# Optimization experiments

Measured on AMD Instinct MI355X. Metric: run time of the kernel, lower is better.

Reference implementation:

```python
import jax, jax.numpy as jnp
import numpy as np


def setup_inputs() -> dict:
    key = jax.random.key(0)
    k1, k2 = jax.random.split(key)
    B, D, NUM_CLASSES = 8192, 128, 100
    features = jax.random.normal(k1, (B, D), dtype=jnp.float32)
    labels = jax.random.randint(k2, (B,), 0, NUM_CLASSES, dtype=jnp.int64)
    return {"features": features, "labels": labels}


def reference(features, labels):
    # temperature=0.07, clamp(min=0.01) -> 0.07
    TEMP = 0.07
    B = features.shape[0]
    dt = features.dtype

    # positive mask from labels: [B, B]
    mask = (labels[:, None] == labels[None, :]).astype(dt)

    # L2 normalize rows (F.normalize: x / max(||x||, eps))
    norm = jnp.sqrt(jnp.sum(features * features, axis=1, keepdims=True))
    f = features / jnp.maximum(norm, 1e-8)

    # similarity matrix, scaled and clamped to [-10, 10]
    sim = jnp.clip(jnp.matmul(f, f.T) / TEMP, -10.0, 10.0)

    eye = jnp.eye(B, dtype=dt)
    exp_sim = jnp.exp(sim)

    pos_sum = jnp.maximum(jnp.sum(exp_sim * (mask - eye), axis=1), 1e-8)
    neg_sum = jnp.maximum(jnp.sum(exp_sim * (1.0 - eye), axis=1), 1e-8)

    loss = -jnp.log(pos_sum / neg_sum)
    # NaN guard as in the original (returns 0 if any NaN)
    return jnp.where(jnp.any(jnp.isnan(loss)), jnp.zeros((), dt), jnp.mean(loss))
```

## Files before the change

### kernel.cpp

```cpp
#include <hip/hip_runtime.h>
#include <hip/hip_bf16.h>


using floatx4 = __attribute__((ext_vector_type(4))) float;
using intx4   = __attribute__((ext_vector_type(4))) int;
using intx8   = __attribute__((ext_vector_type(8))) int;
using llong2  = __attribute__((ext_vector_type(2))) long long;

constexpr int   Bn = 8192;
constexpr int   Dk = 128;
constexpr int   NSLICE = 32;
constexpr int   NBLK   = 32 * 32;
constexpr float PRESCALE = 4.5398160f;
constexpr float LN2      = 0.69314718056f;
constexpr int   SCALE1   = 0x7F7F7F7F;

__global__ __launch_bounds__(256) void normalize_k(
    const float* __restrict__ feat, unsigned char* __restrict__ fb,
    float* __restrict__ rowpos, float* __restrict__ rowneg,
    unsigned int* __restrict__ done) {
  if (blockIdx.x < 32) {
    rowpos[blockIdx.x * 256 + threadIdx.x] = 0.f;
    rowneg[blockIdx.x * 256 + threadIdx.x] = 0.f;
  }
  if (blockIdx.x == 32 && threadIdx.x == 0) *done = 0u;
  const int row  = blockIdx.x * 4 + (threadIdx.x >> 6);
  const int lane = threadIdx.x & 63;
  const float2 v = ((const float2*)(feat + (size_t)row * Dk))[lane];
  float s = v.x * v.x + v.y * v.y;
#pragma unroll
  for (int m = 1; m < 64; m <<= 1) s += __shfl_xor(s, m);
  const float inv = PRESCALE / fmaxf(sqrtf(s), 1e-8f);
  const int packed = __builtin_amdgcn_cvt_pk_fp8_f32(v.x * inv, v.y * inv, 0, false);
  const int k0 = 2 * lane;
  const int p  = ((k0 & 31) >> 3) * 32 + (k0 >> 5) * 8 + (k0 & 7);
  *(unsigned short*)(fb + (size_t)row * Dk + p) = (unsigned short)(packed & 0xffff);
}

__global__ __launch_bounds__(256, 2) void simloss_k(
    const unsigned char* __restrict__ fb, const int* __restrict__ labels,
    float* __restrict__ rowpos, float* __restrict__ rowneg,
    unsigned int* __restrict__ done, float* __restrict__ out) {
  __shared__ __align__(16) unsigned char Bsh[256 * Dk];

  const int t     = threadIdx.x;
  const int lane  = t & 63;
  const int wave  = t >> 6;
  const int quad  = lane >> 4;
  const int lr    = lane & 15;
  const int jbase = blockIdx.x * 256;

  {
    const int chunk = t & 7;
    const int r0    = t >> 3;
#pragma unroll
    for (int it = 0; it < 8; ++it) {
      const int row = r0 + it * 32;
      const llong2 v = *(const llong2*)(fb + (size_t)(jbase + row) * Dk + chunk * 16);
      *(llong2*)(Bsh + row * Dk + ((chunk ^ (row & 7)) * 16)) = v;
    }
  }

  int labj16[8];
#pragma unroll
  for (int j = 0; j < 8; ++j) {
    const int l0 = labels[jbase + (2 * j) * 16 + lr];
    const int l1 = labels[jbase + (2 * j + 1) * 16 + lr];
    labj16[j] = l0 | (l1 << 16);
  }

  bool dl[4];
#pragma unroll
  for (int r = 0; r < 4; ++r) dl[r] = (quad * 4 + r) == lr;

  const int sw  = lr & 7;
  const int ch0 = ((quad * 2)     ^ sw) * 16;
  const int ch1 = ((quad * 2 + 1) ^ sw) * 16;

  __syncthreads();

#pragma unroll 1
  for (int p = 0; p < 2; ++p) {
    const int ibase = blockIdx.y * 256 + wave * 64 + p * 32;

    intx8 A0, A1;
    {
      const unsigned char* ap0 = fb + (size_t)(ibase + lr) * Dk + quad * 32;
      A0 = *(const intx8*)(ap0);
      A1 = *(const intx8*)(ap0 + 16 * Dk);
    }

    int li[2][4];
#pragma unroll
    for (int tt = 0; tt < 2; ++tt)
#pragma unroll
      for (int r = 0; r < 4; ++r)
        li[tt][r] = labels[ibase + tt * 16 + quad * 4 + r];

    float pos[2][4] = {};
    float neg[2][4] = {};

#pragma unroll
    for (int jt = 0; jt < 16; ++jt) {
      const unsigned char* bp = Bsh + (jt * 16 + lr) * Dk;
      const intx4 Blo = *(const intx4*)(bp + ch0);
      const intx4 Bhi = *(const intx4*)(bp + ch1);
      intx8 Bv;
      Bv[0] = Blo[0]; Bv[1] = Blo[1]; Bv[2] = Blo[2]; Bv[3] = Blo[3];
      Bv[4] = Bhi[0]; Bv[5] = Bhi[1]; Bv[6] = Bhi[2]; Bv[7] = Bhi[3];

      floatx4 acc0 = {0.f, 0.f, 0.f, 0.f};
      floatx4 acc1 = {0.f, 0.f, 0.f, 0.f};
      acc0 = __builtin_amdgcn_mfma_scale_f32_16x16x128_f8f6f4(
          A0, Bv, acc0, 0, 0, 0, SCALE1, 0, SCALE1);
      acc1 = __builtin_amdgcn_mfma_scale_f32_16x16x128_f8f6f4(
          A1, Bv, acc1, 0, 0, 0, SCALE1, 0, SCALE1);

      const int j0 = jbase + jt * 16;
      const int lj = (jt & 1) ? (labj16[jt >> 1] >> 16) : (labj16[jt >> 1] & 0xffff);
      float e0, e1, e2, e3;
      e0 = __builtin_amdgcn_exp2f(acc0[0]);
      e1 = __builtin_amdgcn_exp2f(acc0[1]);
      e2 = __builtin_amdgcn_exp2f(acc0[2]);
      e3 = __builtin_amdgcn_exp2f(acc0[3]);
      if (j0 == ibase) {
        if (dl[0]) e0 = 0.f;
        if (dl[1]) e1 = 0.f;
        if (dl[2]) e2 = 0.f;
        if (dl[3]) e3 = 0.f;
      }
      neg[0][0] += e0; neg[0][1] += e1; neg[0][2] += e2; neg[0][3] += e3;
      pos[0][0] += (li[0][0] == lj) ? e0 : 0.f;
      pos[0][1] += (li[0][1] == lj) ? e1 : 0.f;
      pos[0][2] += (li[0][2] == lj) ? e2 : 0.f;
      pos[0][3] += (li[0][3] == lj) ? e3 : 0.f;
      e0 = __builtin_amdgcn_exp2f(acc1[0]);
      e1 = __builtin_amdgcn_exp2f(acc1[1]);
      e2 = __builtin_amdgcn_exp2f(acc1[2]);
      e3 = __builtin_amdgcn_exp2f(acc1[3]);
      if (j0 == ibase + 16) {
        if (dl[0]) e0 = 0.f;
        if (dl[1]) e1 = 0.f;
        if (dl[2]) e2 = 0.f;
        if (dl[3]) e3 = 0.f;
      }
      neg[1][0] += e0; neg[1][1] += e1; neg[1][2] += e2; neg[1][3] += e3;
      pos[1][0] += (li[1][0] == lj) ? e0 : 0.f;
      pos[1][1] += (li[1][1] == lj) ? e1 : 0.f;
      pos[1][2] += (li[1][2] == lj) ? e2 : 0.f;
      pos[1][3] += (li[1][3] == lj) ? e3 : 0.f;
    }

#pragma unroll
    for (int tt = 0; tt < 2; ++tt)
#pragma unroll
      for (int r = 0; r < 4; ++r) {
        float p2 = pos[tt][r], n2 = neg[tt][r];
#pragma unroll
        for (int m = 1; m < 16; m <<= 1) {
          p2 += __shfl_xor(p2, m);
          n2 += __shfl_xor(n2, m);
        }
        if (lr == 0) {
          const int row = ibase + tt * 16 + quad * 4 + r;
          atomicAdd(&rowpos[row], p2);
          atomicAdd(&rowneg[row], n2);
        }
      }

    __builtin_amdgcn_sched_barrier(0);
  }

  __syncthreads();
  int* flag = (int*)Bsh;
  if (t == 0) {
    __threadfence();
    const unsigned int old = atomicAdd(done, 1u);
    *flag = (old == (unsigned)(NBLK - 1)) ? 1 : 0;
  }
  __syncthreads();
  if (*flag) {
    __threadfence();
    const float4* rp4 = (const float4*)rowpos;
    const float4* rn4 = (const float4*)rowneg;
    float4 p4[8], n4[8];
#pragma unroll
    for (int z = 0; z < 8; ++z) p4[z] = rp4[t * 8 + z];
#pragma unroll
    for (int z = 0; z < 8; ++z) n4[z] = rn4[t * 8 + z];
    float acc = 0.f;
#pragma unroll
    for (int z = 0; z < 8; ++z) {
      acc += __builtin_amdgcn_logf(fmaxf(n4[z].x, 1e-8f)) - __builtin_amdgcn_logf(fmaxf(p4[z].x, 1e-8f));
      acc += __builtin_amdgcn_logf(fmaxf(n4[z].y, 1e-8f)) - __builtin_amdgcn_logf(fmaxf(p4[z].y, 1e-8f));
      acc += __builtin_amdgcn_logf(fmaxf(n4[z].z, 1e-8f)) - __builtin_amdgcn_logf(fmaxf(p4[z].z, 1e-8f));
      acc += __builtin_amdgcn_logf(fmaxf(n4[z].w, 1e-8f)) - __builtin_amdgcn_logf(fmaxf(p4[z].w, 1e-8f));
    }
#pragma unroll
    for (int m = 1; m < 64; m <<= 1) acc += __shfl_xor(acc, m);
    float* red = (float*)Bsh + 16;
    if (lane == 0) red[wave] = acc;
    __syncthreads();
    if (t == 0)
      *out = (red[0] + red[1] + red[2] + red[3]) * (LN2 / (float)Bn);
  }
}

extern "C" void kernel_launch(void* const* d_in, const int* in_sizes, int n_in,
                              void* d_out, int out_size, void* d_ws, size_t ws_size,
                              hipStream_t stream) {
  const float* feat   = (const float*)d_in[0];
  const int*   labels = (const int*)d_in[1];
  float* out = (float*)d_out;

  unsigned char* fb = (unsigned char*)d_ws;
  float* rowpos = (float*)((char*)d_ws + (size_t)Bn * Dk);
  float* rowneg = rowpos + Bn;
  unsigned int* done = (unsigned int*)(rowneg + Bn);

  normalize_k<<<Bn / 4, 256, 0, stream>>>(feat, fb, rowpos, rowneg, done);
  dim3 grid(NSLICE, 32);
  simloss_k<<<grid, 256, 0, stream>>>(fb, labels, rowpos, rowneg, done, out);
}
```

Measured before the change: 96.21 us.

## Software-pipeline MFMA with exp epilogue, specialize diagonal blocks, raise occupancy

Restructures the inner tile loop so the next MFMA pair is issued before the previous tile's exp/accumulate epilogue runs, overlapping matrix-core latency with the VALU work. The diagonal-masking logic is moved into a template and compiled only for blocks on the diagonal, so off-diagonal blocks skip the compares. Launch bounds are raised from 2 to 4 blocks per CU for more latency hiding. Keeping both accumulator pairs live costs extra registers, and the higher occupancy target may force spills.

```diff
diff --git a/kernel.cpp b/kernel.cpp
--- a/kernel.cpp
+++ b/kernel.cpp
@@ -37,7 +37,127 @@
   *(unsigned short*)(fb + (size_t)row * Dk + p) = (unsigned short)(packed & 0xffff);
 }
 
-__global__ __launch_bounds__(256, 2) void simloss_k(
+struct Lab16 { int w[8]; };
+
+template <bool DIAG>
+__device__ __forceinline__ void sim_pass(
+    const int ibase, const unsigned char* __restrict__ fb,
+    const int* __restrict__ labels, const unsigned char* __restrict__ Bsh,
+    float* __restrict__ rowpos, float* __restrict__ rowneg,
+    const int jbase, const int quad, const int lr,
+    const int ch0, const int ch1, const Lab16 LJ) {
+
+  intx8 A0, A1;
+  {
+    const unsigned char* ap0 = fb + (size_t)(ibase + lr) * Dk + quad * 32;
+    A0 = *(const intx8*)(ap0);
+    A1 = *(const intx8*)(ap0 + 16 * Dk);
+  }
+
+  int li[2][4];
+#pragma unroll
+  for (int tt = 0; tt < 2; ++tt)
+#pragma unroll
+    for (int r = 0; r < 4; ++r)
+      li[tt][r] = labels[ibase + tt * 16 + quad * 4 + r];
+
+  bool dl[4] = {false, false, false, false};
+  if (DIAG) {
+#pragma unroll
+    for (int r = 0; r < 4; ++r) dl[r] = (quad * 4 + r) == lr;
+  }
+
+  float pos[2][4] = {};
+  float neg[2][4] = {};
+
+  auto loadB = [&](int jt) -> intx8 {
+    const unsigned char* bp = Bsh + (jt * 16 + lr) * Dk;
+    const intx4 Blo = *(const intx4*)(bp + ch0);
+    const intx4 Bhi = *(const intx4*)(bp + ch1);
+    intx8 Bv;
+    Bv[0] = Blo[0]; Bv[1] = Blo[1]; Bv[2] = Blo[2]; Bv[3] = Blo[3];
+    Bv[4] = Bhi[0]; Bv[5] = Bhi[1]; Bv[6] = Bhi[2]; Bv[7] = Bhi[3];
+    return Bv;
+  };
+
+  auto consume = [&](const floatx4 c0, const floatx4 c1, int jt) {
+    const int j0 = jbase + jt * 16;
+    const int lj = (jt & 1) ? (LJ.w[jt >> 1] >> 16) : (LJ.w[jt >> 1] & 0xffff);
+    float e0, e1, e2, e3;
+    e0 = __builtin_amdgcn_exp2f(c0[0]);
+    e1 = __builtin_amdgcn_exp2f(c0[1]);
+    e2 = __builtin_amdgcn_exp2f(c0[2]);
+    e3 = __builtin_amdgcn_exp2f(c0[3]);
+    if (DIAG) {
+      if (j0 == ibase) {
+        if (dl[0]) e0 = 0.f;
+        if (dl[1]) e1 = 0.f;
+        if (dl[2]) e2 = 0.f;
+        if (dl[3]) e3 = 0.f;
+      }
+    }
+    neg[0][0] += e0; neg[0][1] += e1; neg[0][2] += e2; neg[0][3] += e3;
+    pos[0][0] += (li[0][0] == lj) ? e0 : 0.f;
+    pos[0][1] += (li[0][1] == lj) ? e1 : 0.f;
+    pos[0][2] += (li[0][2] == lj) ? e2 : 0.f;
+    pos[0][3] += (li[0][3] == lj) ? e3 : 0.f;
+    e0 = __builtin_amdgcn_exp2f(c1[0]);
+    e1 = __builtin_amdgcn_exp2f(c1[1]);
+    e2 = __builtin_amdgcn_exp2f(c1[2]);
+    e3 = __builtin_amdgcn_exp2f(c1[3]);
+    if (DIAG) {
+      if (j0 == ibase + 16) {
+        if (dl[0]) e0 = 0.f;
+        if (dl[1]) e1 = 0.f;
+        if (dl[2]) e2 = 0.f;
+        if (dl[3]) e3 = 0.f;
+      }
+    }
+    neg[1][0] += e0; neg[1][1] += e1; neg[1][2] += e2; neg[1][3] += e3;
+    pos[1][0] += (li[1][0] == lj) ? e0 : 0.f;
+    pos[1][1] += (li[1][1] == lj) ? e1 : 0.f;
+    pos[1][2] += (li[1][2] == lj) ? e2 : 0.f;
+    pos[1][3] += (li[1][3] == lj) ? e3 : 0.f;
+  };
+
+  const floatx4 z = {0.f, 0.f, 0.f, 0.f};
+
+  intx8 B0 = loadB(0);
+  floatx4 ac0 = __builtin_amdgcn_mfma_scale_f32_16x16x128_f8f6f4(
+      A0, B0, z, 0, 0, 0, SCALE1, 0, SCALE1);
+  floatx4 ac1 = __builtin_amdgcn_mfma_scale_f32_16x16x128_f8f6f4(
+      A1, B0, z, 0, 0, 0, SCALE1, 0, SCALE1);
+#pragma unroll
+  for (int jt = 0; jt < 15; ++jt) {
+    const intx8 Bv = loadB(jt + 1);
+    const floatx4 an0 = __builtin_amdgcn_mfma_scale_f32_16x16x128_f8f6f4(
+        A0, Bv, z, 0, 0, 0, SCALE1, 0, SCALE1);
+    const floatx4 an1 = __builtin_amdgcn_mfma_scale_f32_16x16x128_f8f6f4(
+        A1, Bv, z, 0, 0, 0, SCALE1, 0, SCALE1);
+    consume(ac0, ac1, jt);
+    ac0 = an0; ac1 = an1;
+  }
+  consume(ac0, ac1, 15);
+
+#pragma unroll
+  for (int tt = 0; tt < 2; ++tt)
+#pragma unroll
+    for (int r = 0; r < 4; ++r) {
+      float p2 = pos[tt][r], n2 = neg[tt][r];
+#pragma unroll
+      for (int m = 1; m < 16; m <<= 1) {
+        p2 += __shfl_xor(p2, m);
+        n2 += __shfl_xor(n2, m);
+      }
+      if (lr == 0) {
+        const int row = ibase + tt * 16 + quad * 4 + r;
+        atomicAdd(&rowpos[row], p2);
+        atomicAdd(&rowneg[row], n2);
+      }
+    }
+}
+
+__global__ __launch_bounds__(256, 4) void simloss_k(
     const unsigned char* __restrict__ fb, const int* __restrict__ labels,
     float* __restrict__ rowpos, float* __restrict__ rowneg,
     unsigned int* __restrict__ done, float* __restrict__ out) {
@@ -61,17 +181,13 @@
     }
   }
 
-  int labj16[8];
+  Lab16 LJ;
 #pragma unroll
   for (int j = 0; j < 8; ++j) {
     const int l0 = labels[jbase + (2 * j) * 16 + lr];
     const int l1 = labels[jbase + (2 * j + 1) * 16 + lr];
-    labj16[j] = l0 | (l1 << 16);
-  }
-
-  bool dl[4];
-#pragma unroll
-  for (int r = 0; r < 4; ++r) dl[r] = (quad * 4 + r) == lr;
+    LJ.w[j] = l0 | (l1 << 16);
+  }
 
   const int sw  = lr & 7;
   const int ch0 = ((quad * 2)     ^ sw) * 16;
@@ -79,96 +195,22 @@
 
   __syncthreads();
 
+  const int ib0 = blockIdx.y * 256 + wave * 64;
+
+  if (blockIdx.x == blockIdx.y) {
 #pragma unroll 1
-  for (int p = 0; p < 2; ++p) {
-    const int ibase = blockIdx.y * 256 + wave * 64 + p * 32;
-
-    intx8 A0, A1;
-    {
-      const unsigned char* ap0 = fb + (size_t)(ibase + lr) * Dk + quad * 32;
-      A0 = *(const intx8*)(ap0);
-      A1 = *(const intx8*)(ap0 + 16 * Dk);
-    }
-
-    int li[2][4];
-#pragma unroll
-    for (int tt = 0; tt < 2; ++tt)
-#pragma unroll
-      for (int r = 0; r < 4; ++r)
-        li[tt][r] = labels[ibase + tt * 16 + quad * 4 + r];
-
-    float pos[2][4] = {};
-    float neg[2][4] = {};
-
-#pragma unroll
-    for (int jt = 0; jt < 16; ++jt) {
-      const unsigned char* bp = Bsh + (jt * 16 + lr) * Dk;
-      const intx4 Blo = *(const intx4*)(bp + ch0);
-      const intx4 Bhi = *(const intx4*)(bp + ch1);
-      intx8 Bv;
-      Bv[0] = Blo[0]; Bv[1] = Blo[1]; Bv[2] = Blo[2]; Bv[3] = Blo[3];
-      Bv[4] = Bhi[0]; Bv[5] = Bhi[1]; Bv[6] = Bhi[2]; Bv[7] = Bhi[3];
-
-      floatx4 acc0 = {0.f, 0.f, 0.f, 0.f};
-      floatx4 acc1 = {0.f, 0.f, 0.f, 0.f};
-      acc0 = __builtin_amdgcn_mfma_scale_f32_16x16x128_f8f6f4(
-          A0, Bv, acc0, 0, 0, 0, SCALE1, 0, SCALE1);
-      acc1 = __builtin_amdgcn_mfma_scale_f32_16x16x128_f8f6f4(
-          A1, Bv, acc1, 0, 0, 0, SCALE1, 0, SCALE1);
-
-      const int j0 = jbase + jt * 16;
-      const int lj = (jt & 1) ? (labj16[jt >> 1] >> 16) : (labj16[jt >> 1] & 0xffff);
-      float e0, e1, e2, e3;
-      e0 = __builtin_amdgcn_exp2f(acc0[0]);
-      e1 = __builtin_amdgcn_exp2f(acc0[1]);
-      e2 = __builtin_amdgcn_exp2f(acc0[2]);
-      e3 = __builtin_amdgcn_exp2f(acc0[3]);
-      if (j0 == ibase) {
-        if (dl[0]) e0 = 0.f;
-        if (dl[1]) e1 = 0.f;
-        if (dl[2]) e2 = 0.f;
-        if (dl[3]) e3 = 0.f;
-      }
-      neg[0][0] += e0; neg[0][1] += e1; neg[0][2] += e2; neg[0][3] += e3;
-      pos[0][0] += (li[0][0] == lj) ? e0 : 0.f;
-      pos[0][1] += (li[0][1] == lj) ? e1 : 0.f;
-      pos[0][2] += (li[0][2] == lj) ? e2 : 0.f;
-      pos[0][3] += (li[0][3] == lj) ? e3 : 0.f;
-      e0 = __builtin_amdgcn_exp2f(acc1[0]);
-      e1 = __builtin_amdgcn_exp2f(acc1[1]);
-      e2 = __builtin_amdgcn_exp2f(acc1[2]);
-      e3 = __builtin_amdgcn_exp2f(acc1[3]);
-      if (j0 == ibase + 16) {
-        if (dl[0]) e0 = 0.f;
-        if (dl[1]) e1 = 0.f;
-        if (dl[2]) e2 = 0.f;
-        if (dl[3]) e3 = 0.f;
-      }
-      neg[1][0] += e0; neg[1][1] += e1; neg[1][2] += e2; neg[1][3] += e3;
-      pos[1][0] += (li[1][0] == lj) ? e0 : 0.f;
-      pos[1][1] += (li[1][1] == lj) ? e1 : 0.f;
-      pos[1][2] += (li[1][2] == lj) ? e2 : 0.f;
-      pos[1][3] += (li[1][3] == lj) ? e3 : 0.f;
-    }
-
-#pragma unroll
-    for (int tt = 0; tt < 2; ++tt)
-#pragma unroll
-      for (int r = 0; r < 4; ++r) {
-        float p2 = pos[tt][r], n2 = neg[tt][r];
-#pragma unroll
-        for (int m = 1; m < 16; m <<= 1) {
-          p2 += __shfl_xor(p2, m);
-          n2 += __shfl_xor(n2, m);
-        }
-        if (lr == 0) {
-          const int row = ibase + tt * 16 + quad * 4 + r;
-          atomicAdd(&rowpos[row], p2);
-          atomicAdd(&rowneg[row], n2);
-        }
-      }
-
-    __builtin_amdgcn_sched_barrier(0);
+    for (int p = 0; p < 2; ++p) {
+      sim_pass<true>(ib0 + p * 32, fb, labels, Bsh, rowpos, rowneg,
+                     jbase, quad, lr, ch0, ch1, LJ);
+      __builtin_amdgcn_sched_barrier(0);
+    }
+  } else {
+#pragma unroll 1
+    for (int p = 0; p < 2; ++p) {
+      sim_pass<false>(ib0 + p * 32, fb, labels, Bsh, rowpos, rowneg,
+                      jbase, quad, lr, ch0, ch1, LJ);
+      __builtin_amdgcn_sched_barrier(0);
+    }
   }
 
   __syncthreads();
```

New measurement: 185.8 us. +93.1%, slower.
